# Optimization experiments

Measured on AMD Instinct MI355X. Metric: run time of the kernel, lower is better.

Reference implementation:

```python
import jax, jax.numpy as jnp
import numpy as np

DIM = 1024
HID = 2732  # int(2*4*1024/3) rounded up to multiple of 4
E = 8
TOPK = 2
B, S = 2, 2048


def setup_inputs() -> dict:
    key = jax.random.key(0)
    ks = jax.random.split(key, 5)
    scale = 0.02
    return {
        "x": jax.random.normal(ks[0], (B, S, DIM), dtype=jnp.float32),
        "Wg": jax.random.normal(ks[1], (E, DIM), dtype=jnp.float32) * scale,
        "W1": jax.random.normal(ks[2], (E, HID, DIM), dtype=jnp.float32) * scale,
        "W2": jax.random.normal(ks[3], (E, DIM, HID), dtype=jnp.float32) * scale,
        "W3": jax.random.normal(ks[4], (E, HID, DIM), dtype=jnp.float32) * scale,
    }


def reference(x, Wg, W1, W2, W3):
    b, s, d = x.shape
    xt = x.reshape(b * s, d)                              # [N, d]
    scores = xt @ Wg.T                                    # [N, E]
    w, idx = jax.lax.top_k(scores, TOPK)                  # [N, k]
    w = jax.nn.softmax(w, axis=-1)
    n = xt.shape[0]
    # combine weights scattered back into [N, E] (top-k indices are distinct per row)
    cw = jnp.zeros((n, E), dtype=x.dtype).at[jnp.arange(n)[:, None], idx].set(w)
    # dense per-expert SwiGLU (mathematically identical to masked dispatch)
    h1 = jnp.einsum('nd,ehd->neh', xt, W1)                # [N, E, H]
    h3 = jnp.einsum('nd,ehd->neh', xt, W3)
    h = jax.nn.silu(h1) * h3
    y = jnp.einsum('neh,edh->ned', h, W2)                 # [N, E, d]
    out = jnp.einsum('ned,ne->nd', y, cw)                 # [N, d]
    return out
```

## Files before the change

kernel.cpp:

```cpp
#include <hip/hip_runtime.h>
#include <hip/hip_bf16.h>
#include <stdint.h>

#define DIM   1024
#define HID   2732
#define HPAD  2816
#define NEXP  8
#define NTOK  4096
#define NROW  8192
#define C13BLK 22528

typedef __attribute__((ext_vector_type(8))) short bf16x8;
typedef __attribute__((ext_vector_type(4))) float f32x4;

__device__ __forceinline__ unsigned short f2bf(float f) {
    union { float f; uint32_t u; } v; v.f = f;
    uint32_t u = v.u;
    return (unsigned short)((u + 0x7FFFu + ((u >> 16) & 1u)) >> 16);
}
__device__ __forceinline__ float bf2f(unsigned short h) {
    union { uint32_t u; float f; } v; v.u = ((uint32_t)h) << 16;
    return v.f;
}

#define ASYNC_CP16(g, l) __builtin_amdgcn_global_load_lds( \
    (const __attribute__((address_space(1))) void*)(g), \
    (__attribute__((address_space(3))) void*)(l), 16, 0, 0)

__device__ __forceinline__ void conv13_body(const float* __restrict__ src,
                                            unsigned short* __restrict__ dst, int blk) {
    size_t t = (size_t)blk * 256 + threadIdx.x;
    int d4 = (int)(t & 255);
    size_t rest = t >> 8;
    int hp = (int)(rest % HPAD);
    int e  = (int)(rest / HPAD);
    ushort4 o;
    if (hp < HID) {
        float4 v = *(const float4*)(src + ((size_t)e * HID + hp) * DIM + d4 * 4);
        o.x = f2bf(v.x); o.y = f2bf(v.y); o.z = f2bf(v.z); o.w = f2bf(v.w);
    } else {
        o.x = o.y = o.z = o.w = 0;
    }
    *(ushort4*)(dst + t * 4) = o;
}

__global__ void prep_kernel(const float* __restrict__ x,  const float* __restrict__ Wg,
                            const float* __restrict__ W1, const float* __restrict__ W2,
                            const float* __restrict__ W3,
                            unsigned short* __restrict__ W1b,
                            unsigned short* __restrict__ W2b,
                            unsigned short* __restrict__ W3b,
                            int* __restrict__ counts, int* __restrict__ a_exp,
                            int* __restrict__ a_rank, float* __restrict__ a_w) {
    int b = blockIdx.x;
    if (b < C13BLK) { conv13_body(W1, W1b, b); return; }
    b -= C13BLK;
    if (b < C13BLK) { conv13_body(W3, W3b, b); return; }
    b -= C13BLK;
    if (b < C13BLK) {
        size_t t = (size_t)b * 256 + threadIdx.x;
        int h4 = (int)(t % (HPAD / 4));
        size_t rest = t / (HPAD / 4);
        int d = (int)(rest % DIM);
        int e = (int)(rest / DIM);
        ushort4 o;
        if (h4 * 4 < HID) {
            float4 v = *(const float4*)(W2 + ((size_t)e * DIM + d) * HID + h4 * 4);
            o.x = f2bf(v.x); o.y = f2bf(v.y); o.z = f2bf(v.z); o.w = f2bf(v.w);
        } else {
            o.x = o.y = o.z = o.w = 0;
        }
        *(ushort4*)(W2b + t * 4) = o;
        return;
    }
    b -= C13BLK;
    int wave = threadIdx.x >> 6, lane = threadIdx.x & 63;
    int n = b * 4 + wave;
    const float* xr = x + (size_t)n * DIM + lane * 16;
    float p[NEXP];
#pragma unroll
    for (int e = 0; e < NEXP; ++e) p[e] = 0.f;
#pragma unroll
    for (int i = 0; i < 4; ++i) {
        float4 xv = *(const float4*)(xr + i * 4);
#pragma unroll
        for (int e = 0; e < NEXP; ++e) {
            float4 wv = *(const float4*)(Wg + e * DIM + lane * 16 + i * 4);
            p[e] += xv.x * wv.x + xv.y * wv.y + xv.z * wv.z + xv.w * wv.w;
        }
    }
#pragma unroll
    for (int off = 32; off > 0; off >>= 1)
#pragma unroll
        for (int e = 0; e < NEXP; ++e) p[e] += __shfl_xor(p[e], off);
    if (lane == 0) {
        int i1 = -1, i2 = -1; float m1 = -1e30f, m2 = -1e30f;
#pragma unroll
        for (int e = 0; e < NEXP; ++e) {
            float s = p[e];
            if (s > m1) { m2 = m1; i2 = i1; m1 = s; i1 = e; }
            else if (s > m2) { m2 = s; i2 = e; }
        }
        float e2 = __expf(m2 - m1);
        float inv = 1.f / (1.f + e2);
        int a = n * 2;
        a_exp[a] = i1;  a_w[a] = inv;        a_rank[a] = atomicAdd(&counts[i1], 1);
        a_exp[a+1] = i2; a_w[a+1] = e2 * inv; a_rank[a+1] = atomicAdd(&counts[i2], 1);
    }
}

__global__ void gather_kernel(const float* __restrict__ x, const int* __restrict__ a_exp,
                              const int* __restrict__ a_rank,
                              const int* __restrict__ counts,
                              unsigned short* __restrict__ XG,
                              int* __restrict__ row_of_a) {
    __shared__ int soff[NEXP];
    if (threadIdx.x == 0) {
        int s = 0;
#pragma unroll
        for (int e = 0; e < NEXP; ++e) { soff[e] = s; s += counts[e]; }
    }
    __syncthreads();
    int a = blockIdx.x, n = a >> 1;
    int row = soff[a_exp[a]] + a_rank[a];
    if (threadIdx.x == 0) row_of_a[a] = row;
    float4 xv = *(const float4*)(x + (size_t)n * DIM + threadIdx.x * 4);
    ushort4 o; o.x = f2bf(xv.x); o.y = f2bf(xv.y); o.z = f2bf(xv.z); o.w = f2bf(xv.w);
    *(ushort4*)(XG + (size_t)row * DIM + threadIdx.x * 4) = o;
}

__global__ __launch_bounds__(256, 2) void gemm1_kernel(
    const unsigned short* __restrict__ XG,
    const unsigned short* __restrict__ W1b,
    const unsigned short* __restrict__ W3b,
    const int* __restrict__ counts,
    unsigned short* __restrict__ Hbuf)
{
    const int e = blockIdx.z, mtile = blockIdx.y, ntile = blockIdx.x;
    const int cnt = counts[e];
    if (mtile * 128 >= cnt) return;
    int rowstart = 0;
    for (int i = 0; i < e; ++i) rowstart += counts[i];
    rowstart += mtile * 128;

    __shared__ __align__(16) unsigned short As[128 * 64];
    __shared__ __align__(16) unsigned short B1s[64 * 64];
    __shared__ __align__(16) unsigned short B3s[64 * 64];

    const int tid = threadIdx.x, lane = tid & 63, wave = tid >> 6;
    const int wm = wave >> 1, wn = wave & 1;
    const int quad = lane >> 4;

    const unsigned short* w1e = W1b + (size_t)e * HPAD * DIM;
    const unsigned short* w3e = W3b + (size_t)e * HPAD * DIM;

    const int srow = tid >> 3;
    const int scol = (((tid & 7) ^ (srow & 7)) * 8);
    const unsigned short* ag[4];
#pragma unroll
    for (int r = 0; r < 4; ++r) {
        int grow = rowstart + r * 32 + srow;
        if (grow > NROW - 1) grow = NROW - 1;
        ag[r] = XG + (size_t)grow * DIM + scol;
    }
    const unsigned short* bg1[2]; const unsigned short* bg3[2];
#pragma unroll
    for (int r = 0; r < 2; ++r) {
        int grow = ntile * 64 + r * 32 + srow;
        bg1[r] = w1e + (size_t)grow * DIM + scol;
        bg3[r] = w3e + (size_t)grow * DIM + scol;
    }

    f32x4 acc1[4][2], acc3[4][2];
#pragma unroll
    for (int i = 0; i < 4; ++i)
#pragma unroll
        for (int j = 0; j < 2; ++j) {
            acc1[i][j] = (f32x4){0.f, 0.f, 0.f, 0.f};
            acc3[i][j] = (f32x4){0.f, 0.f, 0.f, 0.f};
        }

    for (int kk = 0; kk < DIM / 64; ++kk) {
        const int k0 = kk * 64;
#pragma unroll
        for (int r = 0; r < 4; ++r)
            ASYNC_CP16(ag[r] + k0, &As[r * 2048 + tid * 8]);
#pragma unroll
        for (int r = 0; r < 2; ++r) {
            ASYNC_CP16(bg1[r] + k0, &B1s[r * 2048 + tid * 8]);
            ASYNC_CP16(bg3[r] + k0, &B3s[r * 2048 + tid * 8]);
        }
        __syncthreads();
#pragma unroll
        for (int ks = 0; ks < 2; ++ks) {
            const int cbase = ks * 4 + quad;
            bf16x8 af[4], b1f[2], b3f[2];
#pragma unroll
            for (int i = 0; i < 4; ++i) {
                int rl = wm * 64 + i * 16 + (lane & 15);
                af[i] = *(const bf16x8*)&As[rl * 64 + ((cbase ^ (rl & 7)) * 8)];
            }
#pragma unroll
            for (int j = 0; j < 2; ++j) {
                int rl1 = wn * 32 + j * 16 + (lane & 15);
                b1f[j] = *(const bf16x8*)&B1s[rl1 * 64 + ((cbase ^ (rl1 & 7)) * 8)];
                b3f[j] = *(const bf16x8*)&B3s[rl1 * 64 + ((cbase ^ (rl1 & 7)) * 8)];
            }
#pragma unroll
            for (int i = 0; i < 4; ++i)
#pragma unroll
                for (int j = 0; j < 2; ++j) {
                    acc1[i][j] = __builtin_amdgcn_mfma_f32_16x16x32_bf16(af[i], b1f[j], acc1[i][j], 0, 0, 0);
                    acc3[i][j] = __builtin_amdgcn_mfma_f32_16x16x32_bf16(af[i], b3f[j], acc3[i][j], 0, 0, 0);
                }
        }
        __syncthreads();
    }

    int mvalid = cnt - mtile * 128; if (mvalid > 128) mvalid = 128;
#pragma unroll
    for (int i = 0; i < 4; ++i)
#pragma unroll
        for (int r = 0; r < 4; ++r) {
            int rl = wm * 64 + i * 16 + quad * 4 + r;
            if (rl < mvalid) {
                size_t rowg = (size_t)(rowstart + rl);
#pragma unroll
                for (int j = 0; j < 2; ++j) {
                    float v1 = acc1[i][j][r], v3 = acc3[i][j][r];
                    float s = v1 / (1.f + __expf(-v1));
                    Hbuf[rowg * HPAD + ntile * 64 + wn * 32 + j * 16 + (lane & 15)] = f2bf(s * v3);
                }
            }
        }
}

__global__ __launch_bounds__(256, 2) void gemm2_kernel(
    const unsigned short* __restrict__ Hbuf,
    const unsigned short* __restrict__ W2b,
    const int* __restrict__ counts,
    unsigned short* __restrict__ Ybuf)
{
    const int e = blockIdx.z, mtile = blockIdx.y, ntile = blockIdx.x;
    const int cnt = counts[e];
    if (mtile * 128 >= cnt) return;
    int rowstart = 0;
    for (int i = 0; i < e; ++i) rowstart += counts[i];
    rowstart += mtile * 128;

    __shared__ __align__(16) unsigned short As[128 * 64];
    __shared__ __align__(16) unsigned short Bs[128 * 64];

    const int tid = threadIdx.x, lane = tid & 63, wave = tid >> 6;
    const int wm = wave >> 1, wn = wave & 1;
    const int quad = lane >> 4;

    const unsigned short* w2e = W2b + (size_t)e * DIM * HPAD;
    const int srow = tid >> 3;
    const int scol = (((tid & 7) ^ (srow & 7)) * 8);
    const unsigned short* ag[4]; const unsigned short* bg[4];
#pragma unroll
    for (int r = 0; r < 4; ++r) {
        int grow = rowstart + r * 32 + srow;
        if (grow > NROW - 1) grow = NROW - 1;
        ag[r] = Hbuf + (size_t)grow * HPAD + scol;
        bg[r] = w2e + (size_t)(ntile * 128 + r * 32 + srow) * HPAD + scol;
    }

    f32x4 acc[4][4];
#pragma unroll
    for (int i = 0; i < 4; ++i)
#pragma unroll
        for (int j = 0; j < 4; ++j) acc[i][j] = (f32x4){0.f, 0.f, 0.f, 0.f};

    for (int kk = 0; kk < HPAD / 64; ++kk) {
        const int k0 = kk * 64;
#pragma unroll
        for (int r = 0; r < 4; ++r) {
            ASYNC_CP16(ag[r] + k0, &As[r * 2048 + tid * 8]);
            ASYNC_CP16(bg[r] + k0, &Bs[r * 2048 + tid * 8]);
        }
        __syncthreads();
#pragma unroll
        for (int ks = 0; ks < 2; ++ks) {
            const int cbase = ks * 4 + quad;
            bf16x8 af[4], bf[4];
#pragma unroll
            for (int i = 0; i < 4; ++i) {
                int rla = wm * 64 + i * 16 + (lane & 15);
                int rlb = wn * 64 + i * 16 + (lane & 15);
                af[i] = *(const bf16x8*)&As[rla * 64 + ((cbase ^ (rla & 7)) * 8)];
                bf[i] = *(const bf16x8*)&Bs[rlb * 64 + ((cbase ^ (rlb & 7)) * 8)];
            }
#pragma unroll
            for (int i = 0; i < 4; ++i)
#pragma unroll
                for (int j = 0; j < 4; ++j)
                    acc[i][j] = __builtin_amdgcn_mfma_f32_16x16x32_bf16(af[i], bf[j], acc[i][j], 0, 0, 0);
        }
        __syncthreads();
    }

    int mvalid = cnt - mtile * 128; if (mvalid > 128) mvalid = 128;
#pragma unroll
    for (int i = 0; i < 4; ++i)
#pragma unroll
        for (int r = 0; r < 4; ++r) {
            int rl = wm * 64 + i * 16 + quad * 4 + r;
            if (rl < mvalid) {
                int rowg = rowstart + rl;
                unsigned short* yrow = Ybuf + (size_t)rowg * DIM + ntile * 128 + wn * 64 + (lane & 15);
#pragma unroll
                for (int j = 0; j < 4; ++j)
                    yrow[j * 16] = f2bf(acc[i][j][r]);
            }
        }
}

__global__ void combine_kernel(const unsigned short* __restrict__ Ybuf,
                               const int* __restrict__ row_of_a,
                               const float* __restrict__ a_w,
                               float* __restrict__ out) {
    int n = blockIdx.x, t = threadIdx.x;
    int r0 = row_of_a[2 * n], r1 = row_of_a[2 * n + 1];
    float w0 = a_w[2 * n], w1 = a_w[2 * n + 1];
    ushort4 y0 = *(const ushort4*)(Ybuf + (size_t)r0 * DIM + t * 4);
    ushort4 y1 = *(const ushort4*)(Ybuf + (size_t)r1 * DIM + t * 4);
    float4 o;
    o.x = w0 * bf2f(y0.x) + w1 * bf2f(y1.x);
    o.y = w0 * bf2f(y0.y) + w1 * bf2f(y1.y);
    o.z = w0 * bf2f(y0.z) + w1 * bf2f(y1.z);
    o.w = w0 * bf2f(y0.w) + w1 * bf2f(y1.w);
    *(float4*)(out + (size_t)n * DIM + t * 4) = o;
}

extern "C" void kernel_launch(void* const* d_in, const int* in_sizes, int n_in,
                              void* d_out, int out_size, void* d_ws, size_t ws_size,
                              hipStream_t stream) {
    const float* x  = (const float*)d_in[0];
    const float* Wg = (const float*)d_in[1];
    const float* W1 = (const float*)d_in[2];
    const float* W2 = (const float*)d_in[3];
    const float* W3 = (const float*)d_in[4];
    float* out = (float*)d_out;

    char* ws = (char*)d_ws;
    size_t off = 0;
    auto alloc = [&](size_t bytes) -> void* {
        void* p = ws + off;
        off = (off + bytes + 255) & ~(size_t)255;
        return p;
    };
    int*   counts      = (int*)alloc(NEXP * 4);
    int*   a_exp       = (int*)alloc(NROW * 4);
    int*   a_rank      = (int*)alloc(NROW * 4);
    float* a_w         = (float*)alloc(NROW * 4);
    int*   row_of_a    = (int*)alloc(NROW * 4);
    unsigned short* XG   = (unsigned short*)alloc((size_t)NROW * DIM * 2);
    unsigned short* Hbuf = (unsigned short*)alloc((size_t)NROW * HPAD * 2);
    unsigned short* W1b  = (unsigned short*)alloc((size_t)NEXP * HPAD * DIM * 2);
    unsigned short* W3b  = (unsigned short*)alloc((size_t)NEXP * HPAD * DIM * 2);
    unsigned short* W2b  = (unsigned short*)alloc((size_t)NEXP * DIM * HPAD * 2);
    unsigned short* Ybuf = (unsigned short*)W1b;

    hipMemsetAsync(counts, 0, NEXP * 4, stream);

    prep_kernel<<<3 * C13BLK + NTOK / 4, 256, 0, stream>>>(
        x, Wg, W1, W2, W3, W1b, W2b, W3b, counts, a_exp, a_rank, a_w);
    gather_kernel<<<NROW, 256, 0, stream>>>(x, a_exp, a_rank, counts, XG, row_of_a);

    gemm1_kernel<<<dim3(HPAD / 64, 64, NEXP), 256, 0, stream>>>(
        XG, W1b, W3b, counts, Hbuf);
    gemm2_kernel<<<dim3(DIM / 128, 64, NEXP), 256, 0, stream>>>(
        Hbuf, W2b, counts, Ybuf);
    combine_kernel<<<NTOK, 256, 0, stream>>>(Ybuf, row_of_a, a_w, out);
}
```

Measured before the change: 574.3 us.

## Fuse fp32-to-bf16 weight conversion into GEMM tile loads, drop prep pass

Removes the separate pass that converted all W1/W3/W2 weights to padded bf16 buffers. The GEMM kernels now read fp32 weights directly, convert them in registers and store them to LDS, prefetching the next k-tile into registers. This avoids writing and re-reading about 138MB of bf16 weights. In exchange, each weight tile is re-read in fp32 (twice the bytes) by every M-tile block, and the async LDS copies for B become synchronous register stores.

```diff
diff --git a/kernel.cpp b/kernel.cpp
--- a/kernel.cpp
+++ b/kernel.cpp
@@ -8,7 +8,6 @@
 #define NEXP  8
 #define NTOK  4096
 #define NROW  8192
-#define C13BLK 22528
 
 typedef __attribute__((ext_vector_type(8))) short bf16x8;
 typedef __attribute__((ext_vector_type(4))) float f32x4;
@@ -27,55 +26,20 @@
     (const __attribute__((address_space(1))) void*)(g), \
     (__attribute__((address_space(3))) void*)(l), 16, 0, 0)
 
-__device__ __forceinline__ void conv13_body(const float* __restrict__ src,
-                                            unsigned short* __restrict__ dst, int blk) {
-    size_t t = (size_t)blk * 256 + threadIdx.x;
-    int d4 = (int)(t & 255);
-    size_t rest = t >> 8;
-    int hp = (int)(rest % HPAD);
-    int e  = (int)(rest / HPAD);
-    ushort4 o;
-    if (hp < HID) {
-        float4 v = *(const float4*)(src + ((size_t)e * HID + hp) * DIM + d4 * 4);
-        o.x = f2bf(v.x); o.y = f2bf(v.y); o.z = f2bf(v.z); o.w = f2bf(v.w);
-    } else {
-        o.x = o.y = o.z = o.w = 0;
-    }
-    *(ushort4*)(dst + t * 4) = o;
-}
-
-__global__ void prep_kernel(const float* __restrict__ x,  const float* __restrict__ Wg,
-                            const float* __restrict__ W1, const float* __restrict__ W2,
-                            const float* __restrict__ W3,
-                            unsigned short* __restrict__ W1b,
-                            unsigned short* __restrict__ W2b,
-                            unsigned short* __restrict__ W3b,
-                            int* __restrict__ counts, int* __restrict__ a_exp,
-                            int* __restrict__ a_rank, float* __restrict__ a_w) {
-    int b = blockIdx.x;
-    if (b < C13BLK) { conv13_body(W1, W1b, b); return; }
-    b -= C13BLK;
-    if (b < C13BLK) { conv13_body(W3, W3b, b); return; }
-    b -= C13BLK;
-    if (b < C13BLK) {
-        size_t t = (size_t)b * 256 + threadIdx.x;
-        int h4 = (int)(t % (HPAD / 4));
-        size_t rest = t / (HPAD / 4);
-        int d = (int)(rest % DIM);
-        int e = (int)(rest / DIM);
-        ushort4 o;
-        if (h4 * 4 < HID) {
-            float4 v = *(const float4*)(W2 + ((size_t)e * DIM + d) * HID + h4 * 4);
-            o.x = f2bf(v.x); o.y = f2bf(v.y); o.z = f2bf(v.z); o.w = f2bf(v.w);
-        } else {
-            o.x = o.y = o.z = o.w = 0;
-        }
-        *(ushort4*)(W2b + t * 4) = o;
-        return;
-    }
-    b -= C13BLK;
+__device__ __forceinline__ bf16x8 pack8(float4 lo, float4 hi, bool vlo, bool vhi) {
+    bf16x8 o;
+    o[0] = (short)(vlo ? f2bf(lo.x) : 0); o[1] = (short)(vlo ? f2bf(lo.y) : 0);
+    o[2] = (short)(vlo ? f2bf(lo.z) : 0); o[3] = (short)(vlo ? f2bf(lo.w) : 0);
+    o[4] = (short)(vhi ? f2bf(hi.x) : 0); o[5] = (short)(vhi ? f2bf(hi.y) : 0);
+    o[6] = (short)(vhi ? f2bf(hi.z) : 0); o[7] = (short)(vhi ? f2bf(hi.w) : 0);
+    return o;
+}
+
+__global__ void route_kernel(const float* __restrict__ x, const float* __restrict__ Wg,
+                             int* __restrict__ counts, int* __restrict__ a_exp,
+                             int* __restrict__ a_rank, float* __restrict__ a_w) {
     int wave = threadIdx.x >> 6, lane = threadIdx.x & 63;
-    int n = b * 4 + wave;
+    int n = blockIdx.x * 4 + wave;
     const float* xr = x + (size_t)n * DIM + lane * 16;
     float p[NEXP];
 #pragma unroll
@@ -131,8 +95,8 @@
 
 __global__ __launch_bounds__(256, 2) void gemm1_kernel(
     const unsigned short* __restrict__ XG,
-    const unsigned short* __restrict__ W1b,
-    const unsigned short* __restrict__ W3b,
+    const float* __restrict__ W1,
+    const float* __restrict__ W3,
     const int* __restrict__ counts,
     unsigned short* __restrict__ Hbuf)
 {
@@ -151,9 +115,6 @@
     const int wm = wave >> 1, wn = wave & 1;
     const int quad = lane >> 4;
 
-    const unsigned short* w1e = W1b + (size_t)e * HPAD * DIM;
-    const unsigned short* w3e = W3b + (size_t)e * HPAD * DIM;
-
     const int srow = tid >> 3;
     const int scol = (((tid & 7) ^ (srow & 7)) * 8);
     const unsigned short* ag[4];
@@ -163,12 +124,14 @@
         if (grow > NROW - 1) grow = NROW - 1;
         ag[r] = XG + (size_t)grow * DIM + scol;
     }
-    const unsigned short* bg1[2]; const unsigned short* bg3[2];
+    bool rv[2]; const float* bg1[2]; const float* bg3[2];
 #pragma unroll
     for (int r = 0; r < 2; ++r) {
         int grow = ntile * 64 + r * 32 + srow;
-        bg1[r] = w1e + (size_t)grow * DIM + scol;
-        bg3[r] = w3e + (size_t)grow * DIM + scol;
+        rv[r] = (grow < HID);
+        int gc = rv[r] ? grow : 0;
+        bg1[r] = W1 + (size_t)e * HID * DIM + (size_t)gc * DIM + scol;
+        bg3[r] = W3 + (size_t)e * HID * DIM + (size_t)gc * DIM + scol;
     }
 
     f32x4 acc1[4][2], acc3[4][2];
@@ -180,6 +143,13 @@
             acc3[i][j] = (f32x4){0.f, 0.f, 0.f, 0.f};
         }
 
+    float4 b1lo[2], b1hi[2], b3lo[2], b3hi[2];
+#pragma unroll
+    for (int r = 0; r < 2; ++r) {
+        b1lo[r] = *(const float4*)(bg1[r]);     b1hi[r] = *(const float4*)(bg1[r] + 4);
+        b3lo[r] = *(const float4*)(bg3[r]);     b3hi[r] = *(const float4*)(bg3[r] + 4);
+    }
+
     for (int kk = 0; kk < DIM / 64; ++kk) {
         const int k0 = kk * 64;
 #pragma unroll
@@ -187,8 +157,16 @@
             ASYNC_CP16(ag[r] + k0, &As[r * 2048 + tid * 8]);
 #pragma unroll
         for (int r = 0; r < 2; ++r) {
-            ASYNC_CP16(bg1[r] + k0, &B1s[r * 2048 + tid * 8]);
-            ASYNC_CP16(bg3[r] + k0, &B3s[r * 2048 + tid * 8]);
+            *(bf16x8*)&B1s[r * 2048 + tid * 8] = pack8(b1lo[r], b1hi[r], rv[r], rv[r]);
+            *(bf16x8*)&B3s[r * 2048 + tid * 8] = pack8(b3lo[r], b3hi[r], rv[r], rv[r]);
+        }
+        if (kk < DIM / 64 - 1) {
+            const int k1 = k0 + 64;
+#pragma unroll
+            for (int r = 0; r < 2; ++r) {
+                b1lo[r] = *(const float4*)(bg1[r] + k1); b1hi[r] = *(const float4*)(bg1[r] + k1 + 4);
+                b3lo[r] = *(const float4*)(bg3[r] + k1); b3hi[r] = *(const float4*)(bg3[r] + k1 + 4);
+            }
         }
         __syncthreads();
 #pragma unroll
@@ -237,7 +215,7 @@
 
 __global__ __launch_bounds__(256, 2) void gemm2_kernel(
     const unsigned short* __restrict__ Hbuf,
-    const unsigned short* __restrict__ W2b,
+    const float* __restrict__ W2,
     const int* __restrict__ counts,
     unsigned short* __restrict__ Ybuf)
 {
@@ -255,16 +233,15 @@
     const int wm = wave >> 1, wn = wave & 1;
     const int quad = lane >> 4;
 
-    const unsigned short* w2e = W2b + (size_t)e * DIM * HPAD;
     const int srow = tid >> 3;
     const int scol = (((tid & 7) ^ (srow & 7)) * 8);
-    const unsigned short* ag[4]; const unsigned short* bg[4];
+    const unsigned short* ag[4]; const float* bg[4];
 #pragma unroll
     for (int r = 0; r < 4; ++r) {
         int grow = rowstart + r * 32 + srow;
         if (grow > NROW - 1) grow = NROW - 1;
         ag[r] = Hbuf + (size_t)grow * HPAD + scol;
-        bg[r] = w2e + (size_t)(ntile * 128 + r * 32 + srow) * HPAD + scol;
+        bg[r] = W2 + (size_t)e * DIM * HID + (size_t)(ntile * 128 + r * 32 + srow) * HID;
     }
 
     f32x4 acc[4][4];
@@ -272,13 +249,33 @@
     for (int i = 0; i < 4; ++i)
 #pragma unroll
         for (int j = 0; j < 4; ++j) acc[i][j] = (f32x4){0.f, 0.f, 0.f, 0.f};
+
+    float4 blo[4], bhi[4];
+#pragma unroll
+    for (int r = 0; r < 4; ++r) {
+        blo[r] = *(const float4*)(bg[r] + scol);
+        bhi[r] = *(const float4*)(bg[r] + scol + 4);
+    }
 
     for (int kk = 0; kk < HPAD / 64; ++kk) {
         const int k0 = kk * 64;
-#pragma unroll
-        for (int r = 0; r < 4; ++r) {
+        const int c = k0 + scol;
+        const bool vlo = (c < HID), vhi = (c + 4 < HID);
+#pragma unroll
+        for (int r = 0; r < 4; ++r)
             ASYNC_CP16(ag[r] + k0, &As[r * 2048 + tid * 8]);
-            ASYNC_CP16(bg[r] + k0, &Bs[r * 2048 + tid * 8]);
+#pragma unroll
+        for (int r = 0; r < 4; ++r)
+            *(bf16x8*)&Bs[r * 2048 + tid * 8] = pack8(blo[r], bhi[r], vlo, vhi);
+        if (kk < HPAD / 64 - 1) {
+            const int cn = c + 64;
+            const int alo = (cn < HID) ? cn : 0;
+            const int ahi = (cn + 4 < HID) ? cn + 4 : 0;
+#pragma unroll
+            for (int r = 0; r < 4; ++r) {
+                blo[r] = *(const float4*)(bg[r] + alo);
+                bhi[r] = *(const float4*)(bg[r] + ahi);
+            }
         }
         __syncthreads();
 #pragma unroll
@@ -358,20 +355,16 @@
     int*   row_of_a    = (int*)alloc(NROW * 4);
     unsigned short* XG   = (unsigned short*)alloc((size_t)NROW * DIM * 2);
     unsigned short* Hbuf = (unsigned short*)alloc((size_t)NROW * HPAD * 2);
-    unsigned short* W1b  = (unsigned short*)alloc((size_t)NEXP * HPAD * DIM * 2);
-    unsigned short* W3b  = (unsigned short*)alloc((size_t)NEXP * HPAD * DIM * 2);
-    unsigned short* W2b  = (unsigned short*)alloc((size_t)NEXP * DIM * HPAD * 2);
-    unsigned short* Ybuf = (unsigned short*)W1b;
+    unsigned short* Ybuf = (unsigned short*)alloc((size_t)NROW * DIM * 2);
 
     hipMemsetAsync(counts, 0, NEXP * 4, stream);
 
-    prep_kernel<<<3 * C13BLK + NTOK / 4, 256, 0, stream>>>(
-        x, Wg, W1, W2, W3, W1b, W2b, W3b, counts, a_exp, a_rank, a_w);
+    route_kernel<<<NTOK / 4, 256, 0, stream>>>(x, Wg, counts, a_exp, a_rank, a_w);
     gather_kernel<<<NROW, 256, 0, stream>>>(x, a_exp, a_rank, counts, XG, row_of_a);
 
     gemm1_kernel<<<dim3(HPAD / 64, 64, NEXP), 256, 0, stream>>>(
-        XG, W1b, W3b, counts, Hbuf);
+        XG, W1, W3, counts, Hbuf);
     gemm2_kernel<<<dim3(DIM / 128, 64, NEXP), 256, 0, stream>>>(
-        Hbuf, W2b, counts, Ybuf);
+        Hbuf, W2, counts, Ybuf);
     combine_kernel<<<NTOK, 256, 0, stream>>>(Ybuf, row_of_a, a_w, out);
 }
```

Result: slower. 610.7 us (+6.3%).
